# Optimization experiments

Measured on AMD Instinct MI355X. Metric: run time of the kernel, lower is better.

## Reference

```python
import jax, jax.numpy as jnp
import numpy as np

H = 16      # headNum
C = 64      # cDim
D = 1024    # qDim = kDim = vDim = outDim
N = 2       # batch
S = 1024    # seq len


def setup_inputs() -> dict:
    key = jax.random.key(0)
    ks = jax.random.split(key, 12)
    inp = {
        "Qin": jax.random.normal(ks[0], (N, S, D), dtype=jnp.float32),
        "Kin": jax.random.normal(ks[1], (N, S, D), dtype=jnp.float32),
        "Vin": jax.random.normal(ks[2], (N, S, D), dtype=jnp.float32),
        "seqMask": jax.random.randint(ks[3], (N, S), 0, 2).astype(jnp.bool_),
        "attMask": jax.random.normal(ks[4], (1, 1, S, S), dtype=jnp.float32),
        # learned parameters (stored as [in, out] for x @ W)
        "QTrans": jax.random.normal(ks[5], (D, H * C), dtype=jnp.float32) * 0.02,
        "KTrans": jax.random.normal(ks[6], (D, H * C), dtype=jnp.float32) * 0.02,
        "VTrans": jax.random.normal(ks[7], (D, H * C), dtype=jnp.float32) * 0.02,
        "GTrans_w": jax.random.normal(ks[8], (D, H * C), dtype=jnp.float32) * 0.02,
        "GTrans_b": jnp.ones((H * C,), dtype=jnp.float32),
        "out_w": jax.random.normal(ks[9], (H * C, D), dtype=jnp.float32) * 0.02,
        "out_b": jnp.zeros((D,), dtype=jnp.float32),
    }
    return inp


def _split_heads(x):
    # [n, s, h*c] -> [h, n, s, c]
    n, s, _ = x.shape
    return x.reshape(n, s, H, C).transpose(2, 0, 1, 3)


def reference(Qin, Kin, Vin, seqMask, attMask, QTrans, KTrans, VTrans,
              GTrans_w, GTrans_b, out_w, out_b):
    Q = _split_heads(Qin @ QTrans)                         # [h,n,s,c]
    K = _split_heads(Kin @ KTrans)                         # [h,n,t,c]
    V = _split_heads(Vin @ VTrans)                         # [h,n,t,c]
    G = jax.nn.sigmoid(_split_heads(Vin @ GTrans_w + GTrans_b))  # [h,n,s,c]

    scale = 1.0 / jnp.sqrt(jnp.float32(C))
    A = jnp.einsum('hnsi,hnti->hnst', Q, K) * scale        # [h,n,s,t]
    # masked_fill where outer-product of seqMask is True
    m = (seqMask[:, :, None] & seqMask[:, None, :])[None]  # [1,n,s,t]
    A = jnp.where(m, -jnp.inf, A)
    A = A + attMask
    A = jax.nn.softmax(A, axis=-1)
    # gated attention-value reduction (eval mode: dropout inactive)
    O = jnp.einsum('hnst,hnti,hnsi->nshi', A, V, G)        # [n,s,h,c]
    O = O.reshape(O.shape[0], O.shape[1], -1)              # [n,s,h*c]
    return O @ out_w + out_b
```

## Files before the change

### kernel.cpp

```cpp
#include <hip/hip_runtime.h>
#include <hip/hip_bf16.h>
#include <cstddef>

#define S_   1024
#define HC_  1024
#define C_   64
#define LOG2E 1.4426950408889634f
#define SC2   0.18033688011112042f

typedef __attribute__((ext_vector_type(8))) short bf16x8;
typedef __attribute__((ext_vector_type(4))) short bf16x4;
typedef __attribute__((ext_vector_type(4))) float f32x4;

typedef __attribute__((address_space(1))) const void gconst_t;
typedef __attribute__((address_space(3))) void lds_t;

__device__ __forceinline__ short cvt_bf16(float f) {
  union { float f; unsigned u; } v; v.f = f;
  unsigned r = v.u + 0x7FFFu + ((v.u >> 16) & 1u);
  return (short)(r >> 16);
}
__device__ __forceinline__ float bf2f(short s) {
  union { float f; unsigned u; } v; v.u = ((unsigned)(unsigned short)s) << 16;
  return v.f;
}

template<int N> __device__ __forceinline__ void wait_vm() {
  if constexpr (N == 0)       asm volatile("s_waitcnt vmcnt(0)" ::: "memory");
  else if constexpr (N == 2)  asm volatile("s_waitcnt vmcnt(2)" ::: "memory");
  else if constexpr (N == 4)  asm volatile("s_waitcnt vmcnt(4)" ::: "memory");
  else if constexpr (N == 6)  asm volatile("s_waitcnt vmcnt(6)" ::: "memory");
  else if constexpr (N == 8)  asm volatile("s_waitcnt vmcnt(8)" ::: "memory");
  else if constexpr (N == 12) asm volatile("s_waitcnt vmcnt(12)" ::: "memory");
}

__global__ __launch_bounds__(256) void prep(
    const float* __restrict__ QT, const float* __restrict__ KT,
    const float* __restrict__ VT, const float* __restrict__ GW,
    const float* __restrict__ OW, short* __restrict__ WTb,
    const float* __restrict__ Qin, const float* __restrict__ Kin,
    const float* __restrict__ Vin, short* __restrict__ Abf,
    const float* __restrict__ att, const unsigned char* __restrict__ sm,
    short* __restrict__ biasP) {
  __shared__ short tile[32][33];
  __shared__ int a1, a4;
  const int bid = blockIdx.x;
  const int t = threadIdx.x;

  if (bid < 5120) {
    const int which = bid >> 10, xb = bid & 1023;
    const float* src = (which == 0) ? QT : (which == 1) ? KT : (which == 2) ? VT
                      : (which == 3) ? GW : OW;
    short* dst = WTb + (size_t)which * (1024u * 1024u);
    const int tj = (xb & 31) * 32;
    const int tk = (xb >> 5) * 32;
    const int r = t >> 3, c4 = (t & 7) * 4;
    const float4 v = *(const float4*)(src + (size_t)(tk + r) * 1024 + tj + c4);
    tile[c4 + 0][r] = cvt_bf16(v.x);
    tile[c4 + 1][r] = cvt_bf16(v.y);
    tile[c4 + 2][r] = cvt_bf16(v.z);
    tile[c4 + 3][r] = cvt_bf16(v.w);
    __syncthreads();
    bf16x4 o;
    o[0] = tile[r][c4 + 0]; o[1] = tile[r][c4 + 1];
    o[2] = tile[r][c4 + 2]; o[3] = tile[r][c4 + 3];
    *(bf16x4*)(dst + (size_t)(tj + r) * 1024 + tk + c4) = o;
  } else if (bid < 8192) {
    const int idx = bid - 5120;
    const int y = idx >> 10, xb = idx & 1023;
    const float* src = (y == 0) ? Qin : (y == 1) ? Kin : Vin;
    short* d = Abf + (size_t)y * 2097152u;
    const int i = (xb * 256 + t) * 8;
    const float4 a = *(const float4*)(src + i);
    const float4 b = *(const float4*)(src + i + 4);
    bf16x8 o;
    o[0] = cvt_bf16(a.x); o[1] = cvt_bf16(a.y); o[2] = cvt_bf16(a.z); o[3] = cvt_bf16(a.w);
    o[4] = cvt_bf16(b.x); o[5] = cvt_bf16(b.y); o[6] = cvt_bf16(b.z); o[7] = cvt_bf16(b.w);
    *(bf16x8*)(d + i) = o;
  } else {
    if (t == 0) { a1 = 0; a4 = 0; }
    __syncthreads();
    int l1 = 0, l4 = 0;
    for (int i = t; i < 2048; i += 256) {
      if (sm[i]) { if (i & 3) l1 = 1; else if (i & 4) l4 = 1; }
    }
    if (l1) atomicOr(&a1, 1);
    if (l4) atomicOr(&a4, 1);
    __syncthreads();
    const int mst = a1 ? 1 : (a4 ? 4 : 8);

    const int idx = bid - 8192;
    const int qw = idx & 63, tt = (idx >> 6) & 15, n = idx >> 10;
    const int lslot = t >> 2, i4 = t & 3;
    const int tc = tt * 64 + i4 * 16 + (lslot & 15);
    const int qbase = qw * 16 + ((lslot >> 4) << 2);
    const int smt = sm[(size_t)(n * 1024 + tc) * mst];
    bf16x4 o;
#pragma unroll
    for (int ii = 0; ii < 4; ii++) {
      const int q = qbase + ii;
      const int smq = sm[(size_t)(n * 1024 + q) * mst];
      const float val = (smq && smt) ? -1e4f : att[(size_t)q * 1024 + tc] * LOG2E;
      o[ii] = cvt_bf16(val);
    }
    short* dst = biasP + (((size_t)(n * 64 + qw) * 16 + tt) * 64 + lslot) * 16 + i4 * 4;
    *(bf16x4*)dst = o;
  }
}

template<int MW, int NW>
__device__ __forceinline__ void gemm_core_bf(
    const short* __restrict__ A, const short* __restrict__ BT,
    short* As, short* Bs, int m0, int n0, f32x4 acc[MW][NW]) {
  const int t = threadIdx.x;
  const int lane = t & 63, wid = t >> 6;
  const int wr = wid >> 1, wc = wid & 1;
  const int l15 = lane & 15, g = lane >> 4;
  constexpr int NT = 32;
  constexpr int LDT = MW / 2 + NW / 2;
  constexpr int ABUF = MW * 1024;
  constexpr int BBUF = NW * 1024;

#pragma unroll
  for (int m = 0; m < MW; m++)
#pragma unroll
    for (int n2 = 0; n2 < NW; n2++) acc[m][n2] = (f32x4){0.f, 0.f, 0.f, 0.f};

#define STAGE_(buf, kt)                                                        \
  {                                                                            \
    const int k0_ = (kt) * 32;                                                 \
    _Pragma("unroll")                                                          \
    for (int i_ = 0; i_ < NW / 2; i_++) {                                      \
      const int seg_ = i_ * 256 + t;                                           \
      const int row_ = seg_ >> 2, gl_ = seg_ & 3;                              \
      __builtin_amdgcn_global_load_lds(                                        \
          (gconst_t*)(BT + (size_t)(n0 + row_) * 1024 + k0_ +                  \
                      ((gl_ ^ ((row_ >> 1) & 3)) * 8)),                        \
          (lds_t*)(Bs + (buf) * BBUF + seg_ * 8), 16, 0, 0);                   \
    }                                                                          \
    _Pragma("unroll")                                                          \
    for (int i_ = 0; i_ < MW / 2; i_++) {                                      \
      const int seg_ = i_ * 256 + t;                                           \
      const int row_ = seg_ >> 2, gl_ = seg_ & 3;                              \
      __builtin_amdgcn_global_load_lds(                                        \
          (gconst_t*)(A + (size_t)(m0 + row_) * 1024 + k0_ +                   \
                      ((gl_ ^ ((row_ >> 1) & 3)) * 8)),                        \
          (lds_t*)(As + (buf) * ABUF + seg_ * 8), 16, 0, 0);                   \
    }                                                                          \
  }

  STAGE_(0, 0);
  STAGE_(1, 1);
  STAGE_(2, 2);
  int b0 = 0, b1 = 1, b2 = 2, b3 = 3;
  for (int kt = 0; kt < NT; ++kt) {
    if (kt + 3 < NT) {
      STAGE_(b3, kt + 3);
      wait_vm<3 * LDT>();
    } else if (kt + 3 == NT) {
      wait_vm<2 * LDT>();
    } else if (kt + 2 == NT) {
      wait_vm<LDT>();
    } else {
      wait_vm<0>();
    }
    __builtin_amdgcn_sched_barrier(0);
    __builtin_amdgcn_s_barrier();
    __builtin_amdgcn_sched_barrier(0);

    const short* Ac = As + b0 * ABUF;
    const short* Bc = Bs + b0 * BBUF;
    bf16x8 a[MW], b[NW];
#pragma unroll
    for (int m = 0; m < MW; m++) {
      const int row = wr * (MW * 16) + m * 16 + l15;
      a[m] = *(const bf16x8*)(Ac + row * 32 + ((g ^ ((row >> 1) & 3)) * 8));
    }
#pragma unroll
    for (int n2 = 0; n2 < NW; n2++) {
      const int row = wc * (NW * 16) + n2 * 16 + l15;
      b[n2] = *(const bf16x8*)(Bc + row * 32 + ((g ^ ((row >> 1) & 3)) * 8));
    }
    __builtin_amdgcn_s_setprio(1);
#pragma unroll
    for (int m = 0; m < MW; m++)
#pragma unroll
      for (int n2 = 0; n2 < NW; n2++)
        acc[m][n2] = __builtin_amdgcn_mfma_f32_16x16x32_bf16(a[m], b[n2], acc[m][n2], 0, 0, 0);
    __builtin_amdgcn_s_setprio(0);
    __builtin_amdgcn_sched_barrier(0);
    __builtin_amdgcn_s_barrier();
    __builtin_amdgcn_sched_barrier(0);
    const int tmp = b0; b0 = b1; b1 = b2; b2 = b3; b3 = tmp;
  }
#undef STAGE_
}

__global__ __launch_bounds__(256) void gemm_proj(
    const short* __restrict__ Abf, const short* __restrict__ WTb,
    short* __restrict__ Pb, short* __restrict__ VpT,
    const float* __restrict__ gb) {
  __shared__ short As[4 * 4096];
  __shared__ short Bs[4 * 4096];
  const int bid = blockIdx.x;
  const int xcd = bid & 7, ord = bid >> 3;
  const int y = xcd >> 1, nh = xcd & 1;
  const int m0 = (ord & 15) * 128;
  const int n0 = (nh * 4 + (ord >> 4)) * 128;
  const short* A = Abf + (size_t)((y <= 2) ? y : 2) * 2097152u;
  const short* BT = WTb + (size_t)y * (1024u * 1024u);
  f32x4 acc[4][4];
  gemm_core_bf<4, 4>(A, BT, As, Bs, m0, n0, acc);
  const int t = threadIdx.x, lane = t & 63, wid = t >> 6;
  const int wr = wid >> 1, wc = wid & 1, l15 = lane & 15, g = lane >> 4;

  if (y == 2) {
    short* Tr = As;
#pragma unroll
    for (int m = 0; m < 4; m++)
#pragma unroll
      for (int n2 = 0; n2 < 4; n2++)
#pragma unroll
        for (int j = 0; j < 4; j++) {
          const int r = wr * 64 + m * 16 + g * 4 + j;
          const int c = wc * 64 + n2 * 16 + l15;
          Tr[c * 128 + r] = cvt_bf16(acc[m][n2][j]);
        }
    __syncthreads();
    const int nz = (m0 >= 1024) ? 1 : 0;
    const int sbase = m0 & 1023;
#pragma unroll
    for (int p = 0; p < 8; p++) {
      const int unit = p * 256 + t;
      const int cl = unit >> 4, sr8 = unit & 15;
      const bf16x8 v = *(const bf16x8*)(Tr + cl * 128 + sr8 * 8);
      *(bf16x8*)(VpT + ((size_t)(nz * 1024 + n0 + cl)) * 1024 + sbase + sr8 * 8) = v;
    }
  } else {
    short* outp = Pb + (size_t)y * 2097152u;
#pragma unroll
    for (int m = 0; m < 4; m++)
#pragma unroll
      for (int n2 = 0; n2 < 4; n2++)
#pragma unroll
        for (int j = 0; j < 4; j++) {
          const int row = m0 + wr * 64 + m * 16 + g * 4 + j;
          const int col = n0 + wc * 64 + n2 * 16 + l15;
          float v = acc[m][n2][j];
          if (y == 3) { v += gb[col]; v = 1.0f / (1.0f + __expf(-v)); }
          outp[(size_t)row * 1024 + col] = cvt_bf16(v);
        }
  }
}

__global__ __launch_bounds__(256) void gemm_final(
    const short* __restrict__ Aobuf, const short* __restrict__ WTo,
    float* __restrict__ outp, const float* __restrict__ ob) {
  __shared__ short As[4 * 2048];
  __shared__ short Bs[4 * 2048];
  const int bid = blockIdx.x;
  const int xcd = bid & 7, ord = bid >> 3;
  const int mg = xcd >> 1, ng = xcd & 1;
  const int m0 = (mg * 8 + (ord & 7)) * 64;
  const int n0 = (ng * 8 + (ord >> 3)) * 64;
  f32x4 acc[2][2];
  gemm_core_bf<2, 2>(Aobuf, WTo, As, Bs, m0, n0, acc);
  const int t = threadIdx.x, lane = t & 63, wid = t >> 6;
  const int wr = wid >> 1, wc = wid & 1, l15 = lane & 15, g = lane >> 4;
#pragma unroll
  for (int m = 0; m < 2; m++)
#pragma unroll
    for (int n2 = 0; n2 < 2; n2++)
#pragma unroll
      for (int j = 0; j < 4; j++) {
        const int row = m0 + wr * 32 + m * 16 + g * 4 + j;
        const int col = n0 + wc * 32 + n2 * 16 + l15;
        outp[(size_t)row * 1024 + col] = acc[m][n2][j] + ob[col];
      }
}

__global__ __launch_bounds__(256) void attn_split(
    const short* __restrict__ Qp, const short* __restrict__ Kp,
    const short* __restrict__ VpT, const short* __restrict__ biasP,
    float* __restrict__ mlbuf, short* __restrict__ OpartB, int lns) {
  __shared__ short Ks[64 * 64];
  __shared__ short Vt[64 * 64];
  __shared__ short Pl[4][16 * 64];

  const int t = threadIdx.x;
  const int lane = t & 63, w = t >> 6;
  const int l15 = lane & 15, g = lane >> 4;
  const int xb = blockIdx.x, h = blockIdx.y, n = blockIdx.z;
  const int sp = xb & ((1 << lns) - 1), qb = xb >> lns;
  const int itc = 16 >> lns;

  const int sbase = qb * 64 + w * 16;
  const short* qptr = Qp + (size_t)(n * S_ + sbase + l15) * HC_ + h * C_;
  const bf16x8 qf0 = *(const bf16x8*)(qptr + g * 8);
  const bf16x8 qf1 = *(const bf16x8*)(qptr + 32 + g * 8);

  float mrow[4], lsum[4];
  f32x4 oacc[4];
#pragma unroll
  for (int j = 0; j < 4; j++) { mrow[j] = -1e30f; lsum[j] = 0.f; }
#pragma unroll
  for (int cb = 0; cb < 4; cb++) oacc[cb] = (f32x4){0.f, 0.f, 0.f, 0.f};

  const int str = t >> 3, sc8 = (t & 7) * 8;
  const short* bbase = biasP + ((size_t)(n * 64 + qb * 4 + w) * 16 * 64 + lane) * 16;

  {
    const int t0 = sp * itc * 64;
    bf16x8 kA0 = *(const bf16x8*)(Kp + (size_t)(n * S_ + t0 + str) * HC_ + h * C_ + sc8);
    bf16x8 kA1 = *(const bf16x8*)(Kp + (size_t)(n * S_ + t0 + 32 + str) * HC_ + h * C_ + sc8);
    bf16x8 vA0 = *(const bf16x8*)(VpT + ((size_t)n * HC_ + h * C_ + str) * S_ + t0 + sc8);
    bf16x8 vA1 = *(const bf16x8*)(VpT + ((size_t)n * HC_ + h * C_ + 32 + str) * S_ + t0 + sc8);

    for (int it = 0; it < itc; ++it) {
      const int tg = sp * itc + it;
      __syncthreads();
      { const int kr = str;      *(bf16x8*)((char*)Ks + kr * 128 + ((sc8 * 2) ^ ((kr & 7) << 4))) = kA0; }
      { const int kr = 32 + str; *(bf16x8*)((char*)Ks + kr * 128 + ((sc8 * 2) ^ ((kr & 7) << 4))) = kA1; }
      { const int cr = str;      *(bf16x8*)((char*)Vt + cr * 128 + ((sc8 * 2) ^ ((cr & 7) << 4))) = vA0; }
      { const int cr = 32 + str; *(bf16x8*)((char*)Vt + cr * 128 + ((sc8 * 2) ^ ((cr & 7) << 4))) = vA1; }
      __syncthreads();

      const bf16x8 bf0 = *(const bf16x8*)(bbase + tg * 1024);
      const bf16x8 bf1 = *(const bf16x8*)(bbase + tg * 1024 + 8);
      const int t1 = ((it + 1 < itc) ? (tg + 1) : tg) * 64;
      bf16x8 kB0 = *(const bf16x8*)(Kp + (size_t)(n * S_ + t1 + str) * HC_ + h * C_ + sc8);
      bf16x8 kB1 = *(const bf16x8*)(Kp + (size_t)(n * S_ + t1 + 32 + str) * HC_ + h * C_ + sc8);
      bf16x8 vB0 = *(const bf16x8*)(VpT + ((size_t)n * HC_ + h * C_ + str) * S_ + t1 + sc8);
      bf16x8 vB1 = *(const bf16x8*)(VpT + ((size_t)n * HC_ + h * C_ + 32 + str) * S_ + t1 + sc8);

      f32x4 sacc[4];
#pragma unroll
      for (int nb = 0; nb < 4; nb++) sacc[nb] = (f32x4){0.f, 0.f, 0.f, 0.f};
      __builtin_amdgcn_s_setprio(1);
#pragma unroll
      for (int nb = 0; nb < 4; nb++) {
        const int krow = nb * 16 + l15;
        const bf16x8 b0 = *(const bf16x8*)((char*)Ks + krow * 128 + ((g * 16) ^ ((krow & 7) << 4)));
        const bf16x8 b1 = *(const bf16x8*)((char*)Ks + krow * 128 + ((64 + g * 16) ^ ((krow & 7) << 4)));
        sacc[nb] = __builtin_amdgcn_mfma_f32_16x16x32_bf16(qf0, b0, sacc[nb], 0, 0, 0);
        sacc[nb] = __builtin_amdgcn_mfma_f32_16x16x32_bf16(qf1, b1, sacc[nb], 0, 0, 0);
      }
      __builtin_amdgcn_s_setprio(0);

      float tmax[4];
#pragma unroll
      for (int j = 0; j < 4; j++) tmax[j] = -1e30f;
#pragma unroll
      for (int nb = 0; nb < 4; nb++)
#pragma unroll
        for (int j = 0; j < 4; j++) {
          const short bb = (nb < 2) ? bf0[nb * 4 + j] : bf1[(nb - 2) * 4 + j];
          const float lg = sacc[nb][j] * SC2 + bf2f(bb);
          sacc[nb][j] = lg;
          tmax[j] = fmaxf(tmax[j], lg);
        }
#pragma unroll
      for (int j = 0; j < 4; j++) {
#pragma unroll
        for (int d = 1; d < 16; d <<= 1)
          tmax[j] = fmaxf(tmax[j], __shfl_xor(tmax[j], d, 64));
        const float mn = fmaxf(mrow[j], tmax[j]);
        const float sc = exp2f(mrow[j] - mn);
        mrow[j] = mn;
        lsum[j] *= sc;
#pragma unroll
        for (int cb = 0; cb < 4; cb++) oacc[cb][j] *= sc;
        float ps = 0.f;
#pragma unroll
        for (int nb = 0; nb < 4; nb++) {
          const float p = exp2f(sacc[nb][j] - mn);
          sacc[nb][j] = p;
          ps += p;
        }
        lsum[j] += ps;
      }
      short* Pw = &Pl[w][0];
#pragma unroll
      for (int nb = 0; nb < 4; nb++)
#pragma unroll
        for (int j = 0; j < 4; j++) {
          const int pr = g * 4 + j;
          const int pcb = (nb * 16 + l15) * 2;
          *(short*)((char*)Pw + pr * 128 + (pcb ^ ((pr & 7) << 4))) = cvt_bf16(sacc[nb][j]);
        }
      __builtin_amdgcn_s_setprio(1);
#pragma unroll
      for (int kk = 0; kk < 2; kk++) {
        const bf16x8 pf = *(const bf16x8*)((char*)Pw + l15 * 128 + ((kk * 64 + g * 16) ^ ((l15 & 7) << 4)));
#pragma unroll
        for (int cb = 0; cb < 4; cb++) {
          const int vrow = cb * 16 + l15;
          const bf16x8 vf = *(const bf16x8*)((char*)Vt + vrow * 128 + ((kk * 64 + g * 16) ^ ((vrow & 7) << 4)));
          oacc[cb] = __builtin_amdgcn_mfma_f32_16x16x32_bf16(pf, vf, oacc[cb], 0, 0, 0);
        }
      }
      __builtin_amdgcn_s_setprio(0);
      kA0 = kB0; kA1 = kB1; vA0 = vB0; vA1 = vB1;
    }
  }
  const int slot = (((n * 16 + h) * 16 + qb) << lns) + sp;
  short* op = OpartB + (size_t)slot * 4096;
  float* mlp = mlbuf + (size_t)slot * 128;
#pragma unroll
  for (int j = 0; j < 4; j++) {
    float rs = lsum[j];
#pragma unroll
    for (int d = 1; d < 16; d <<= 1) rs += __shfl_xor(rs, d, 64);
    const int row = w * 16 + g * 4 + j;
#pragma unroll
    for (int cb = 0; cb < 4; cb++)
      op[row * 64 + cb * 16 + l15] = cvt_bf16(oacc[cb][j]);
    if (l15 == 0) { mlp[row * 2] = mrow[j]; mlp[row * 2 + 1] = rs; }
  }
}

__global__ __launch_bounds__(256) void attn_merge(
    const short* __restrict__ OpartB, const float* __restrict__ mlbuf,
    const short* __restrict__ Gp, short* __restrict__ ObufB, int lns) {
  const int qb = blockIdx.x, h = blockIdx.y, n = blockIdx.z;
  const int nsplit = 1 << lns;
  const int t = threadIdx.x;
  const int r = t >> 2, c0 = (t & 3) * 16;
  const int bslot = ((n * 16 + h) * 16 + qb) << lns;
  const float* mlb = mlbuf + (size_t)bslot * 128 + r * 2;

  float M = -1e30f;
  for (int sp = 0; sp < nsplit; sp++) M = fmaxf(M, mlb[(size_t)sp * 128]);
  float l = 0.f;
  for (int sp = 0; sp < nsplit; sp++)
    l += exp2f(mlb[(size_t)sp * 128] - M) * mlb[(size_t)sp * 128 + 1];
  const float inv = 1.0f / l;

  float acc[16];
#pragma unroll
  for (int k = 0; k < 16; k++) acc[k] = 0.f;
  for (int sp = 0; sp < nsplit; sp++) {
    const float wsc = exp2f(mlb[(size_t)sp * 128] - M);
    const short* op = OpartB + (size_t)(bslot + sp) * 4096 + r * 64 + c0;
    const bf16x8 v0 = *(const bf16x8*)(op);
    const bf16x8 v1 = *(const bf16x8*)(op + 8);
#pragma unroll
    for (int k = 0; k < 8; k++) {
      acc[k]     += wsc * bf2f(v0[k]);
      acc[8 + k] += wsc * bf2f(v1[k]);
    }
  }
  const int srow = qb * 64 + r;
  const size_t idx = (size_t)(n * S_ + srow) * HC_ + h * C_ + c0;
  const bf16x8 g0 = *(const bf16x8*)(Gp + idx);
  const bf16x8 g1 = *(const bf16x8*)(Gp + idx + 8);
  bf16x8 o0, o1;
#pragma unroll
  for (int k = 0; k < 8; k++) {
    o0[k] = cvt_bf16(acc[k] * inv * bf2f(g0[k]));
    o1[k] = cvt_bf16(acc[8 + k] * inv * bf2f(g1[k]));
  }
  *(bf16x8*)(ObufB + idx) = o0;
  *(bf16x8*)(ObufB + idx + 8) = o1;
}

extern "C" void kernel_launch(void* const* d_in, const int* in_sizes, int n_in,
                              void* d_out, int out_size, void* d_ws, size_t ws_size,
                              hipStream_t stream) {
  const float* Qin      = (const float*)d_in[0];
  const float* Kin      = (const float*)d_in[1];
  const float* Vin      = (const float*)d_in[2];
  const void*  seqMask  = d_in[3];
  const float* attMask  = (const float*)d_in[4];
  const float* QTrans   = (const float*)d_in[5];
  const float* KTrans   = (const float*)d_in[6];
  const float* VTrans   = (const float*)d_in[7];
  const float* GTrans_w = (const float*)d_in[8];
  const float* GTrans_b = (const float*)d_in[9];
  const float* out_w    = (const float*)d_in[10];
  const float* out_b    = (const float*)d_in[11];
  float* out = (float*)d_out;

  char* ws = (char*)d_ws;
  const size_t MB = 1048576u;
  short* WTb   = (short*)(ws);
  short* Abf   = (short*)(ws + 10 * MB);
  short* Pb    = (short*)(ws + 22 * MB);
  short* VpT   = (short*)(ws + 38 * MB);
  short* ObufB = (short*)(ws + 42 * MB);
  short* biasP = (short*)(ws + 46 * MB);
  const size_t partBase = 51 * MB;

  const short* Kp = Pb + (size_t)1u * 2097152u;
  const short* Gp = Pb + (size_t)3u * 2097152u;

  int lns = 0;
  for (int c = 1; c >= 0; c--) {
    const size_t slots = 512u << c;
    if (ws_size >= partBase + slots * (8192u + 512u)) { lns = c; break; }
  }
  const size_t slots = 512u << lns;
  short* OpartB = (short*)(ws + partBase);
  float* mlbuf  = (float*)(ws + partBase + slots * 8192u);

  hipLaunchKernelGGL(prep, dim3(10240), dim3(256), 0, stream,
                     QTrans, KTrans, VTrans, GTrans_w, out_w, WTb,
                     Qin, Kin, Vin, Abf,
                     attMask, (const unsigned char*)seqMask, biasP);
  hipLaunchKernelGGL(gemm_proj, dim3(512), dim3(256), 0, stream,
                     Abf, WTb, Pb, VpT, GTrans_b);
  hipLaunchKernelGGL(attn_split, dim3(16 << lns, 16, 2), dim3(256), 0, stream,
                     Pb, Kp, VpT, biasP, mlbuf, OpartB, lns);
  hipLaunchKernelGGL(attn_merge, dim3(16, 16, 2), dim3(256), 0, stream,
                     OpartB, mlbuf, Gp, ObufB, lns);
  hipLaunchKernelGGL(gemm_final, dim3(512), dim3(256), 0, stream,
                     ObufB, WTb + (size_t)4u * 1048576u, out, out_b);
}
```

Measured before the change: 112.2 us.

## Replace LDS-staged GEMM pipeline with direct global-to-register MFMA loads

The 4-stage global_load_lds pipeline with barriers is removed from both projection and final GEMMs. Each wave now loads its MFMA fragments straight from global memory into registers in a fully unrolled K loop, relying on L1/L2 for reuse instead of shared memory. The final GEMM also moves to 64x128 tiles with half as many blocks. This drops barrier and LDS traffic, but costs redundant global loads across waves, loses explicit prefetch depth, and may raise register pressure.

Measured after the change: 153.8 us. 1.37x slower.

```diff
diff --git a/kernel.cpp b/kernel.cpp
--- a/kernel.cpp
+++ b/kernel.cpp
@@ -12,9 +12,6 @@
 typedef __attribute__((ext_vector_type(4))) short bf16x4;
 typedef __attribute__((ext_vector_type(4))) float f32x4;
 
-typedef __attribute__((address_space(1))) const void gconst_t;
-typedef __attribute__((address_space(3))) void lds_t;
-
 __device__ __forceinline__ short cvt_bf16(float f) {
   union { float f; unsigned u; } v; v.f = f;
   unsigned r = v.u + 0x7FFFu + ((v.u >> 16) & 1u);
@@ -23,15 +20,6 @@
 __device__ __forceinline__ float bf2f(short s) {
   union { float f; unsigned u; } v; v.u = ((unsigned)(unsigned short)s) << 16;
   return v.f;
-}
-
-template<int N> __device__ __forceinline__ void wait_vm() {
-  if constexpr (N == 0)       asm volatile("s_waitcnt vmcnt(0)" ::: "memory");
-  else if constexpr (N == 2)  asm volatile("s_waitcnt vmcnt(2)" ::: "memory");
-  else if constexpr (N == 4)  asm volatile("s_waitcnt vmcnt(4)" ::: "memory");
-  else if constexpr (N == 6)  asm volatile("s_waitcnt vmcnt(6)" ::: "memory");
-  else if constexpr (N == 8)  asm volatile("s_waitcnt vmcnt(8)" ::: "memory");
-  else if constexpr (N == 12) asm volatile("s_waitcnt vmcnt(12)" ::: "memory");
 }
 
 __global__ __launch_bounds__(256) void prep(
@@ -109,78 +97,37 @@
 }
 
 template<int MW, int NW>
-__device__ __forceinline__ void gemm_core_bf(
+__device__ __forceinline__ void gemm_direct(
     const short* __restrict__ A, const short* __restrict__ BT,
-    short* As, short* Bs, int m0, int n0, f32x4 acc[MW][NW]) {
+    int m0, int n0, f32x4 acc[MW][NW]) {
   const int t = threadIdx.x;
   const int lane = t & 63, wid = t >> 6;
   const int wr = wid >> 1, wc = wid & 1;
   const int l15 = lane & 15, g = lane >> 4;
-  constexpr int NT = 32;
-  constexpr int LDT = MW / 2 + NW / 2;
-  constexpr int ABUF = MW * 1024;
-  constexpr int BBUF = NW * 1024;
-
+
+  const short* ap[MW];
+  const short* bp[NW];
 #pragma unroll
   for (int m = 0; m < MW; m++)
+    ap[m] = A + (size_t)(m0 + wr * (MW * 16) + m * 16 + l15) * 1024 + g * 8;
+#pragma unroll
+  for (int n2 = 0; n2 < NW; n2++)
+    bp[n2] = BT + (size_t)(n0 + wc * (NW * 16) + n2 * 16 + l15) * 1024 + g * 8;
+
+#pragma unroll
+  for (int m = 0; m < MW; m++)
 #pragma unroll
     for (int n2 = 0; n2 < NW; n2++) acc[m][n2] = (f32x4){0.f, 0.f, 0.f, 0.f};
 
-#define STAGE_(buf, kt)                                                        \
-  {                                                                            \
-    const int k0_ = (kt) * 32;                                                 \
-    _Pragma("unroll")                                                          \
-    for (int i_ = 0; i_ < NW / 2; i_++) {                                      \
-      const int seg_ = i_ * 256 + t;                                           \
-      const int row_ = seg_ >> 2, gl_ = seg_ & 3;                              \
-      __builtin_amdgcn_global_load_lds(                                        \
-          (gconst_t*)(BT + (size_t)(n0 + row_) * 1024 + k0_ +                  \
-                      ((gl_ ^ ((row_ >> 1) & 3)) * 8)),                        \
-          (lds_t*)(Bs + (buf) * BBUF + seg_ * 8), 16, 0, 0);                   \
-    }                                                                          \
-    _Pragma("unroll")                                                          \
-    for (int i_ = 0; i_ < MW / 2; i_++) {                                      \
-      const int seg_ = i_ * 256 + t;                                           \
-      const int row_ = seg_ >> 2, gl_ = seg_ & 3;                              \
-      __builtin_amdgcn_global_load_lds(                                        \
-          (gconst_t*)(A + (size_t)(m0 + row_) * 1024 + k0_ +                   \
-                      ((gl_ ^ ((row_ >> 1) & 3)) * 8)),                        \
-          (lds_t*)(As + (buf) * ABUF + seg_ * 8), 16, 0, 0);                   \
-    }                                                                          \
-  }
-
-  STAGE_(0, 0);
-  STAGE_(1, 1);
-  STAGE_(2, 2);
-  int b0 = 0, b1 = 1, b2 = 2, b3 = 3;
-  for (int kt = 0; kt < NT; ++kt) {
-    if (kt + 3 < NT) {
-      STAGE_(b3, kt + 3);
-      wait_vm<3 * LDT>();
-    } else if (kt + 3 == NT) {
-      wait_vm<2 * LDT>();
-    } else if (kt + 2 == NT) {
-      wait_vm<LDT>();
-    } else {
-      wait_vm<0>();
-    }
-    __builtin_amdgcn_sched_barrier(0);
-    __builtin_amdgcn_s_barrier();
-    __builtin_amdgcn_sched_barrier(0);
-
-    const short* Ac = As + b0 * ABUF;
-    const short* Bc = Bs + b0 * BBUF;
+#pragma unroll
+  for (int kt = 0; kt < 32; ++kt) {
     bf16x8 a[MW], b[NW];
 #pragma unroll
-    for (int m = 0; m < MW; m++) {
-      const int row = wr * (MW * 16) + m * 16 + l15;
-      a[m] = *(const bf16x8*)(Ac + row * 32 + ((g ^ ((row >> 1) & 3)) * 8));
-    }
-#pragma unroll
-    for (int n2 = 0; n2 < NW; n2++) {
-      const int row = wc * (NW * 16) + n2 * 16 + l15;
-      b[n2] = *(const bf16x8*)(Bc + row * 32 + ((g ^ ((row >> 1) & 3)) * 8));
-    }
+    for (int m = 0; m < MW; m++)
+      a[m] = *(const bf16x8*)(ap[m] + kt * 32);
+#pragma unroll
+    for (int n2 = 0; n2 < NW; n2++)
+      b[n2] = *(const bf16x8*)(bp[n2] + kt * 32);
     __builtin_amdgcn_s_setprio(1);
 #pragma unroll
     for (int m = 0; m < MW; m++)
@@ -188,20 +135,14 @@
       for (int n2 = 0; n2 < NW; n2++)
         acc[m][n2] = __builtin_amdgcn_mfma_f32_16x16x32_bf16(a[m], b[n2], acc[m][n2], 0, 0, 0);
     __builtin_amdgcn_s_setprio(0);
-    __builtin_amdgcn_sched_barrier(0);
-    __builtin_amdgcn_s_barrier();
-    __builtin_amdgcn_sched_barrier(0);
-    const int tmp = b0; b0 = b1; b1 = b2; b2 = b3; b3 = tmp;
-  }
-#undef STAGE_
+  }
 }
 
 __global__ __launch_bounds__(256) void gemm_proj(
     const short* __restrict__ Abf, const short* __restrict__ WTb,
     short* __restrict__ Pb, short* __restrict__ VpT,
     const float* __restrict__ gb) {
-  __shared__ short As[4 * 4096];
-  __shared__ short Bs[4 * 4096];
+  __shared__ short Tr[128 * 128];
   const int bid = blockIdx.x;
   const int xcd = bid & 7, ord = bid >> 3;
   const int y = xcd >> 1, nh = xcd & 1;
@@ -210,12 +151,11 @@
   const short* A = Abf + (size_t)((y <= 2) ? y : 2) * 2097152u;
   const short* BT = WTb + (size_t)y * (1024u * 1024u);
   f32x4 acc[4][4];
-  gemm_core_bf<4, 4>(A, BT, As, Bs, m0, n0, acc);
+  gemm_direct<4, 4>(A, BT, m0, n0, acc);
   const int t = threadIdx.x, lane = t & 63, wid = t >> 6;
   const int wr = wid >> 1, wc = wid & 1, l15 = lane & 15, g = lane >> 4;
 
   if (y == 2) {
-    short* Tr = As;
 #pragma unroll
     for (int m = 0; m < 4; m++)
 #pragma unroll
@@ -256,25 +196,22 @@
 __global__ __launch_bounds__(256) void gemm_final(
     const short* __restrict__ Aobuf, const short* __restrict__ WTo,
     float* __restrict__ outp, const float* __restrict__ ob) {
-  __shared__ short As[4 * 2048];
-  __shared__ short Bs[4 * 2048];
   const int bid = blockIdx.x;
   const int xcd = bid & 7, ord = bid >> 3;
-  const int mg = xcd >> 1, ng = xcd & 1;
-  const int m0 = (mg * 8 + (ord & 7)) * 64;
-  const int n0 = (ng * 8 + (ord >> 3)) * 64;
-  f32x4 acc[2][2];
-  gemm_core_bf<2, 2>(Aobuf, WTo, As, Bs, m0, n0, acc);
+  const int m0 = (xcd * 4 + (ord & 3)) * 64;
+  const int n0 = (ord >> 2) * 128;
+  f32x4 acc[2][4];
+  gemm_direct<2, 4>(Aobuf, WTo, m0, n0, acc);
   const int t = threadIdx.x, lane = t & 63, wid = t >> 6;
   const int wr = wid >> 1, wc = wid & 1, l15 = lane & 15, g = lane >> 4;
 #pragma unroll
   for (int m = 0; m < 2; m++)
 #pragma unroll
-    for (int n2 = 0; n2 < 2; n2++)
+    for (int n2 = 0; n2 < 4; n2++)
 #pragma unroll
       for (int j = 0; j < 4; j++) {
         const int row = m0 + wr * 32 + m * 16 + g * 4 + j;
-        const int col = n0 + wc * 32 + n2 * 16 + l15;
+        const int col = n0 + wc * 64 + n2 * 16 + l15;
         outp[(size_t)row * 1024 + col] = acc[m][n2][j] + ob[col];
       }
 }
@@ -513,6 +450,6 @@
                      Pb, Kp, VpT, biasP, mlbuf, OpartB, lns);
   hipLaunchKernelGGL(attn_merge, dim3(16, 16, 2), dim3(256), 0, stream,
                      OpartB, mlbuf, Gp, ObufB, lns);
-  hipLaunchKernelGGL(gemm_final, dim3(512), dim3(256), 0, stream,
+  hipLaunchKernelGGL(gemm_final, dim3(256), dim3(256), 0, stream,
                      ObufB, WTb + (size_t)4u * 1048576u, out, out_b);
 }
```
